# Kernel tuning notes

Measured on AMD Instinct MI355X. Metric: run time of the kernel, lower is better.

## Reference

```python
import jax, jax.numpy as jnp
import numpy as np

N_NUM = 100        # numerical columns
N_CAT = 100        # categorical columns
CAT_COUNT = 100    # categories per categorical column
N_COND = 128
EPS = 1e-5         # torch GroupNorm default eps


def setup_inputs() -> dict:
    key = jax.random.key(0)
    ks = jax.random.split(key, 8)
    B = 4096
    return {
        "x_num": jax.random.normal(ks[0], (B, N_NUM), dtype=jnp.float32),
        "x_cat": jax.random.randint(ks[1], (B, N_CAT), 0, CAT_COUNT),
        "W_num": jax.random.normal(ks[2], (N_NUM, N_COND), dtype=jnp.float32),
        "b_num": jax.random.normal(ks[3], (N_NUM, N_COND), dtype=jnp.float32),
        "emb_table": jax.random.normal(ks[4], (N_CAT * CAT_COUNT, N_COND), dtype=jnp.float32),
        "gn_w": jnp.ones((N_CAT, N_COND), dtype=jnp.float32),
        "gn_b": jnp.zeros((N_CAT, N_COND), dtype=jnp.float32),
        "W_cat": jax.random.normal(ks[5], (N_CAT, N_COND, N_COND), dtype=jnp.float32) / np.sqrt(N_COND).astype(np.float32),
        "b_cat": jax.random.normal(ks[6], (N_CAT, N_COND), dtype=jnp.float32),
    }


def reference(x_num, x_cat, W_num, b_num, emb_table, gn_w, gn_b, W_cat, b_cat):
    # --- numerical branch: grouped 1x1 conv (Cin/g=1, Cout/g=n_cond) + sigmoid ---
    # (B, n_num, 1) * (n_num, n_cond) + bias -> (B, n_num, n_cond)
    num_emb = jax.nn.sigmoid(x_num[:, :, None] * W_num[None] + b_num[None])

    # --- categorical branch ---
    offsets = jnp.arange(N_CAT, dtype=x_cat.dtype) * CAT_COUNT  # cat_offset
    emb = emb_table[x_cat + offsets[None]]  # (B, n_cat, n_cond)

    # GroupNorm with n_cat groups over n_cat*n_cond channels (spatial dim = 1):
    # normalize each column's n_cond features per sample (biased variance).
    mean = jnp.mean(emb, axis=-1, keepdims=True)
    var = jnp.var(emb, axis=-1, keepdims=True)
    normed = (emb - mean) * jax.lax.rsqrt(var + EPS)
    normed = normed * gn_w[None] + gn_b[None]

    # grouped 1x1 conv, groups = n_cat: per-column n_cond x n_cond matmul
    cat_emb = jax.nn.sigmoid(jnp.einsum('bgi,gio->bgo', normed, W_cat) + b_cat[None])

    M = jnp.concatenate([num_emb, cat_emb], axis=1)  # (B, n_num+n_cat, n_cond)
    return jnp.transpose(M, (0, 2, 1))               # (B, n_cond, n_num+n_cat)
```

## Files before the change

kernel.cpp:

```cpp
#include <hip/hip_runtime.h>
#include <cstdint>

#define NNUM 100
#define NCAT 100
#define CATC 100
#define NCOND 128
#define GN_EPS 1e-5f

typedef __attribute__((ext_vector_type(8))) short bfrag8;
typedef __attribute__((ext_vector_type(4))) float accf4;

__device__ __forceinline__ float sigmoidf_(float x) { return 1.0f / (1.0f + __expf(-x)); }

__device__ __forceinline__ ushort f2bf(float f) {
    uint32_t u = __builtin_bit_cast(uint32_t, f);
    u += 0x7fffu + ((u >> 16) & 1u);
    return (ushort)(u >> 16);
}
__device__ __forceinline__ float bf2f(ushort h) {
    return __builtin_bit_cast(float, (uint32_t)h << 16);
}

__global__ __launch_bounds__(256)
void prep_wcat(const float* __restrict__ W_cat, const float* __restrict__ gn_w,
               ushort* __restrict__ Wf)
{
    const int g    = blockIdx.x;
    const int lane = threadIdx.x & 63;
    const int w    = threadIdx.x >> 6;
    const float* Wg = W_cat + ((size_t)g << 14);
    const float* gwg = gn_w + g * NCOND;
    ushort* Wfg = Wf + ((size_t)g << 15);
    #pragma unroll
    for (int i = 0; i < 8; ++i) {
        int p  = w * 8 + i;
        int t  = p >> 2, kk = p & 3;
        int c  = t * 16 + (lane & 15);
        int kb = kk * 32 + ((lane >> 4) << 3);
        ushort hi[8], lo[8];
        #pragma unroll
        for (int j = 0; j < 8; ++j) {
            float v = gwg[kb + j] * Wg[(kb + j) * NCOND + c];
            ushort h = f2bf(v);
            hi[j] = h;
            lo[j] = f2bf(v - bf2f(h));
        }
        int off = ((t * 4 + kk) * 2) * 512 + lane * 8;
        *(bfrag8*)(Wfg + off)       = *(const bfrag8*)hi;
        *(bfrag8*)(Wfg + off + 512) = *(const bfrag8*)lo;
    }
}

__global__ __launch_bounds__(256)
void prep_stats(const float* __restrict__ emb_table, float2* __restrict__ S)
{
    int r = blockIdx.x * 4 + (threadIdx.x >> 6);
    int lane = threadIdx.x & 63;
    if (r >= NCAT * CATC) return;
    const float2* row = (const float2*)(emb_table + ((size_t)r << 7));
    float2 v = row[lane];
    float s  = v.x + v.y;
    float ss = v.x * v.x + v.y * v.y;
    #pragma unroll
    for (int off = 32; off > 0; off >>= 1) {
        s  += __shfl_xor(s,  off, 64);
        ss += __shfl_xor(ss, off, 64);
    }
    float mean = s * 0.0078125f;
    float var  = fmaf(-mean, mean, ss * 0.0078125f);
    float rs   = rsqrtf(var + GN_EPS);
    if (lane == 0) S[r] = make_float2(rs, -mean * rs);
}

__global__ __launch_bounds__(128)
void prep_qp(const float* __restrict__ W_cat, const float* __restrict__ gn_w,
             const float* __restrict__ gn_b, const float* __restrict__ b_cat,
             float* __restrict__ Q, float* __restrict__ P)
{
    const int g = blockIdx.x, o = threadIdx.x;
    const float* Wg = W_cat + ((size_t)g << 14);
    float q = 0.f, p = 0.f;
    #pragma unroll 4
    for (int i = 0; i < NCOND; ++i) {
        float wv = Wg[i * NCOND + o];
        q = fmaf(gn_w[g * NCOND + i], wv, q);
        p = fmaf(gn_b[g * NCOND + i], wv, p);
    }
    Q[g * NCOND + o] = q;
    P[g * NCOND + o] = p + b_cat[g * NCOND + o];
}

__global__ __launch_bounds__(256, 2)
void prep_E_kernel(const float* __restrict__ emb_table,
                   const ushort* __restrict__ Wf,
                   float* __restrict__ E)
{
    const int g    = blockIdx.x;
    const int tid  = threadIdx.x;
    const int lane = tid & 63;
    const int w    = tid >> 6;

    __shared__ __align__(16) ushort Ahi[128 * 128];
    __shared__ __align__(16) ushort Alo[128 * 128];

    const int half = lane >> 5;
    const int l5   = lane & 31;

    #pragma unroll 8
    for (int it = 0; it < 16; ++it) {
        int r = it * 2 + half;
        int m = w * 32 + r;
        int row_id = m < CATC ? m : (CATC - 1);
        const float4* row = (const float4*)(emb_table + ((size_t)(g * CATC + row_id) << 7));
        float4 v = row[l5];
        ushort h0 = f2bf(v.x), h1 = f2bf(v.y), h2 = f2bf(v.z), h3 = f2bf(v.w);
        uint2 hp = { (uint32_t)h0 | ((uint32_t)h1 << 16),
                     (uint32_t)h2 | ((uint32_t)h3 << 16) };
        uint2 lp = { (uint32_t)f2bf(v.x - bf2f(h0)) | ((uint32_t)f2bf(v.y - bf2f(h1)) << 16),
                     (uint32_t)f2bf(v.z - bf2f(h2)) | ((uint32_t)f2bf(v.w - bf2f(h3)) << 16) };
        int bo = m * 256 + ((l5 * 8) ^ ((m & 7) << 4));
        *(uint2*)((char*)Ahi + bo) = hp;
        *(uint2*)((char*)Alo + bo) = lp;
    }
    asm volatile("s_waitcnt lgkmcnt(0)" ::: "memory");

    accf4 acc[2][8];
    #pragma unroll
    for (int gi = 0; gi < 2; ++gi)
        #pragma unroll
        for (int t = 0; t < 8; ++t)
            acc[gi][t] = (accf4){0.f, 0.f, 0.f, 0.f};

    const ushort* Wfg = Wf + ((size_t)g << 15);
    const int row0 = w * 32 + (lane & 15);
    const int sw   = (lane & 7) << 4;

    #pragma unroll
    for (int kk = 0; kk < 4; ++kk) {
        int colb = kk * 64 + ((lane >> 4) << 4);
        int o0 = row0 * 256 + (colb ^ sw);
        int o1 = o0 + 16 * 256;
        bfrag8 ah0 = *(const bfrag8*)((const char*)Ahi + o0);
        bfrag8 al0 = *(const bfrag8*)((const char*)Alo + o0);
        bfrag8 ah1 = *(const bfrag8*)((const char*)Ahi + o1);
        bfrag8 al1 = *(const bfrag8*)((const char*)Alo + o1);
        const ushort* wbase = Wfg + kk * 1024 + lane * 8;
        #pragma unroll
        for (int t = 0; t < 8; ++t) {
            bfrag8 wh = *(const bfrag8*)(wbase + t * 4096);
            bfrag8 wl = *(const bfrag8*)(wbase + t * 4096 + 512);
            acc[0][t] = __builtin_amdgcn_mfma_f32_16x16x32_bf16(ah0, wh, acc[0][t], 0, 0, 0);
            acc[0][t] = __builtin_amdgcn_mfma_f32_16x16x32_bf16(ah0, wl, acc[0][t], 0, 0, 0);
            acc[0][t] = __builtin_amdgcn_mfma_f32_16x16x32_bf16(al0, wh, acc[0][t], 0, 0, 0);
            acc[0][t] = __builtin_amdgcn_mfma_f32_16x16x32_bf16(al0, wl, acc[0][t], 0, 0, 0);
            acc[1][t] = __builtin_amdgcn_mfma_f32_16x16x32_bf16(ah1, wh, acc[1][t], 0, 0, 0);
            acc[1][t] = __builtin_amdgcn_mfma_f32_16x16x32_bf16(ah1, wl, acc[1][t], 0, 0, 0);
            acc[1][t] = __builtin_amdgcn_mfma_f32_16x16x32_bf16(al1, wh, acc[1][t], 0, 0, 0);
            acc[1][t] = __builtin_amdgcn_mfma_f32_16x16x32_bf16(al1, wl, acc[1][t], 0, 0, 0);
        }
    }

    float* Eg = E + (size_t)g * (CATC * NCOND);
    const int colL = lane & 15;
    const int quad = lane >> 4;
    #pragma unroll
    for (int t = 0; t < 8; ++t) {
        int c = t * 16 + colL;
        #pragma unroll
        for (int gi = 0; gi < 2; ++gi) {
            int mbase = (2 * w + gi) * 16 + quad * 4;
            #pragma unroll
            for (int r = 0; r < 4; ++r) {
                int m = mbase + r;
                if (m < CATC) Eg[m * NCOND + c] = acc[gi][t][r];
            }
        }
    }
}

__global__ __launch_bounds__(256)
void transpose_wn(const float* __restrict__ W_num, const float* __restrict__ b_num,
                  float* __restrict__ Wt, float* __restrict__ Bt)
{
    int idx = blockIdx.x * 256 + threadIdx.x;
    if (idx < NCOND * NNUM) {
        int c = idx / NNUM, j = idx - c * NNUM;
        Wt[idx] = W_num[j * NCOND + c];
        Bt[idx] = b_num[j * NCOND + c];
    }
}

__global__ __launch_bounds__(256)
void fused_out_kernel(const int* __restrict__ x_cat,
                      const float* __restrict__ x_num,
                      const float* __restrict__ Wt,
                      const float* __restrict__ Bt,
                      const float* __restrict__ Q,
                      const float* __restrict__ P,
                      const float2* __restrict__ S,
                      const float* __restrict__ E,
                      float* __restrict__ out)
{
    const int b   = blockIdx.x;
    const int h   = blockIdx.y;
    const int tid = threadIdx.x;
    __shared__ float T[NCAT * 65];
    __shared__ float xr[NNUM];
    __shared__ float al[NCAT], be[NCAT];
    __shared__ int   ei[NCAT];

    if (tid < NNUM) xr[tid] = x_num[b * NNUM + tid];
    if (tid < NCAT) {
        int idx = x_cat[(size_t)b * NCAT + tid];
        ei[tid] = idx;
        float2 s2 = S[tid * CATC + idx];
        al[tid] = s2.x;
        be[tid] = s2.y;
    }
    __syncthreads();

    const float4* E4 = (const float4*)E;
    const float4* Q4 = (const float4*)Q;
    const float4* P4 = (const float4*)P;
    #pragma unroll
    for (int it = 0; it < 7; ++it) {
        int i4 = it * 256 + tid;
        if (i4 < NCAT * 16) {
            int g    = i4 >> 4;
            int c4   = i4 & 15;
            int col4 = h * 16 + c4;
            float4 e = E4[(size_t)(g * CATC + ei[g]) * 32 + col4];
            float4 q = Q4[g * 32 + col4];
            float4 p = P4[g * 32 + col4];
            float a = al[g], bb = be[g];
            float* d = &T[g * 65 + c4 * 4];
            d[0] = sigmoidf_(fmaf(a, e.x, fmaf(bb, q.x, p.x)));
            d[1] = sigmoidf_(fmaf(a, e.y, fmaf(bb, q.y, p.y)));
            d[2] = sigmoidf_(fmaf(a, e.z, fmaf(bb, q.z, p.z)));
            d[3] = sigmoidf_(fmaf(a, e.w, fmaf(bb, q.w, p.w)));
        }
    }
    __syncthreads();

    float4* outb = (float4*)(out + (size_t)b * (NCOND * 200)) + h * 3200;
    const float4* Wt4 = (const float4*)Wt;
    const float4* Bt4 = (const float4*)Bt;
    #pragma unroll
    for (int it = 0; it < 13; ++it) {
        int o4 = it * 256 + tid;
        if (o4 < 64 * 50) {
            int c_loc = o4 / 50;
            int j4    = o4 - c_loc * 50;
            int c     = h * 64 + c_loc;
            float4 v;
            if (j4 < 25) {
                float4 wv = Wt4[c * 25 + j4];
                float4 bv = Bt4[c * 25 + j4];
                int j = j4 * 4;
                v.x = sigmoidf_(fmaf(xr[j],     wv.x, bv.x));
                v.y = sigmoidf_(fmaf(xr[j + 1], wv.y, bv.y));
                v.z = sigmoidf_(fmaf(xr[j + 2], wv.z, bv.z));
                v.w = sigmoidf_(fmaf(xr[j + 3], wv.w, bv.w));
            } else {
                int gg = (j4 - 25) * 4;
                v.x = T[(gg    ) * 65 + c_loc];
                v.y = T[(gg + 1) * 65 + c_loc];
                v.z = T[(gg + 2) * 65 + c_loc];
                v.w = T[(gg + 3) * 65 + c_loc];
            }
            outb[o4] = v;
        }
    }
}

extern "C" void kernel_launch(void* const* d_in, const int* in_sizes, int n_in,
                              void* d_out, int out_size, void* d_ws, size_t ws_size,
                              hipStream_t stream)
{
    const float* x_num  = (const float*)d_in[0];
    const int*   x_cat  = (const int*)  d_in[1];
    const float* W_num  = (const float*)d_in[2];
    const float* b_num  = (const float*)d_in[3];
    const float* emb    = (const float*)d_in[4];
    const float* gn_w   = (const float*)d_in[5];
    const float* gn_b   = (const float*)d_in[6];
    const float* W_cat  = (const float*)d_in[7];
    const float* b_cat  = (const float*)d_in[8];
    float* out = (float*)d_out;

    const int B = in_sizes[0] / NNUM;

    float*  Wt = (float*)d_ws;
    float*  Bt = Wt + NCOND * NNUM;
    float*  Qb = Bt + NCOND * NNUM;
    float*  Pb = Qb + NCAT * NCOND;
    float2* Sb = (float2*)(Pb + NCAT * NCOND);
    float*  Eb = (float*)(Sb + NCAT * CATC);
    ushort* Wf = (ushort*)(Eb + NCAT * CATC * NCOND);

    transpose_wn<<<(NCOND * NNUM + 255) / 256, 256, 0, stream>>>(W_num, b_num, Wt, Bt);
    prep_wcat<<<NCAT, 256, 0, stream>>>(W_cat, gn_w, Wf);
    prep_stats<<<(NCAT * CATC + 3) / 4, 256, 0, stream>>>(emb, Sb);
    prep_qp<<<NCAT, 128, 0, stream>>>(W_cat, gn_w, gn_b, b_cat, Qb, Pb);
    prep_E_kernel<<<NCAT, 256, 0, stream>>>(emb, Wf, Eb);
    fused_out_kernel<<<dim3(B, 2), 256, 0, stream>>>(x_cat, x_num, Wt, Bt, Qb, Pb, Sb, Eb, out);
}
```

Measured before the change: 513.4 us.

## Fuse all prep kernels into one and restructure output tile layout

Merges the five preprocessing kernels (W_num transpose, W_cat bf16 split, row stats, Q/P vectors, E matmul) into one launch. The gn_w scaling moves onto the embedding operand, and Q/P come out as two extra MFMA rows, with W_cat split in shared memory in two K-chunks. The output kernel now stores the categorical tile transposed with padding, so the final copy uses float4 shared-memory reads, and it writes numerical and categorical halves in separate loops. This removes several launches and the Wf round trip, at the cost of more per-block work and shared memory in the fused prep kernel.

```diff
diff --git a/kernel.cpp b/kernel.cpp
--- a/kernel.cpp
+++ b/kernel.cpp
@@ -22,141 +22,135 @@
 }
 
 __global__ __launch_bounds__(256)
-void prep_wcat(const float* __restrict__ W_cat, const float* __restrict__ gn_w,
-               ushort* __restrict__ Wf)
+void prep_all(const float* __restrict__ emb_table,
+              const float* __restrict__ W_cat,
+              const float* __restrict__ gn_w,
+              const float* __restrict__ gn_b,
+              const float* __restrict__ b_cat,
+              const float* __restrict__ W_num,
+              const float* __restrict__ b_num,
+              float* __restrict__ E, float* __restrict__ Q, float* __restrict__ P,
+              float2* __restrict__ S,
+              float* __restrict__ Wt, float* __restrict__ Bt)
 {
+    const int tid  = threadIdx.x;
+
+    if (blockIdx.x >= NCAT) {
+        int idx = (blockIdx.x - NCAT) * 256 + tid;
+        if (idx < NCOND * NNUM) {
+            int c = idx / NNUM, j = idx - c * NNUM;
+            Wt[idx] = W_num[j * NCOND + c];
+            Bt[idx] = b_num[j * NCOND + c];
+        }
+        return;
+    }
+
     const int g    = blockIdx.x;
-    const int lane = threadIdx.x & 63;
-    const int w    = threadIdx.x >> 6;
-    const float* Wg = W_cat + ((size_t)g << 14);
-    const float* gwg = gn_w + g * NCOND;
-    ushort* Wfg = Wf + ((size_t)g << 15);
-    #pragma unroll
-    for (int i = 0; i < 8; ++i) {
-        int p  = w * 8 + i;
-        int t  = p >> 2, kk = p & 3;
-        int c  = t * 16 + (lane & 15);
-        int kb = kk * 32 + ((lane >> 4) << 3);
-        ushort hi[8], lo[8];
-        #pragma unroll
-        for (int j = 0; j < 8; ++j) {
-            float v = gwg[kb + j] * Wg[(kb + j) * NCOND + c];
-            ushort h = f2bf(v);
-            hi[j] = h;
-            lo[j] = f2bf(v - bf2f(h));
-        }
-        int off = ((t * 4 + kk) * 2) * 512 + lane * 8;
-        *(bfrag8*)(Wfg + off)       = *(const bfrag8*)hi;
-        *(bfrag8*)(Wfg + off + 512) = *(const bfrag8*)lo;
-    }
-}
-
-__global__ __launch_bounds__(256)
-void prep_stats(const float* __restrict__ emb_table, float2* __restrict__ S)
-{
-    int r = blockIdx.x * 4 + (threadIdx.x >> 6);
-    int lane = threadIdx.x & 63;
-    if (r >= NCAT * CATC) return;
-    const float2* row = (const float2*)(emb_table + ((size_t)r << 7));
-    float2 v = row[lane];
-    float s  = v.x + v.y;
-    float ss = v.x * v.x + v.y * v.y;
-    #pragma unroll
-    for (int off = 32; off > 0; off >>= 1) {
-        s  += __shfl_xor(s,  off, 64);
-        ss += __shfl_xor(ss, off, 64);
-    }
-    float mean = s * 0.0078125f;
-    float var  = fmaf(-mean, mean, ss * 0.0078125f);
-    float rs   = rsqrtf(var + GN_EPS);
-    if (lane == 0) S[r] = make_float2(rs, -mean * rs);
-}
-
-__global__ __launch_bounds__(128)
-void prep_qp(const float* __restrict__ W_cat, const float* __restrict__ gn_w,
-             const float* __restrict__ gn_b, const float* __restrict__ b_cat,
-             float* __restrict__ Q, float* __restrict__ P)
-{
-    const int g = blockIdx.x, o = threadIdx.x;
-    const float* Wg = W_cat + ((size_t)g << 14);
-    float q = 0.f, p = 0.f;
-    #pragma unroll 4
-    for (int i = 0; i < NCOND; ++i) {
-        float wv = Wg[i * NCOND + o];
-        q = fmaf(gn_w[g * NCOND + i], wv, q);
-        p = fmaf(gn_b[g * NCOND + i], wv, p);
-    }
-    Q[g * NCOND + o] = q;
-    P[g * NCOND + o] = p + b_cat[g * NCOND + o];
-}
-
-__global__ __launch_bounds__(256, 2)
-void prep_E_kernel(const float* __restrict__ emb_table,
-                   const ushort* __restrict__ Wf,
-                   float* __restrict__ E)
-{
-    const int g    = blockIdx.x;
-    const int tid  = threadIdx.x;
     const int lane = tid & 63;
     const int w    = tid >> 6;
 
-    __shared__ __align__(16) ushort Ahi[128 * 128];
-    __shared__ __align__(16) ushort Alo[128 * 128];
-
+    __shared__ __align__(16) ushort Ahi[128 * 64];
+    __shared__ __align__(16) ushort Alo[128 * 64];
+    __shared__ __align__(16) ushort Wc[2][8192];
+
+    const float2* emb2 = (const float2*)emb_table;
+    #pragma unroll 5
+    for (int i = 0; i < 25; ++i) {
+        int m = w + 4 * i;
+        float2 v = emb2[(size_t)(g * CATC + m) * 64 + lane];
+        float s  = v.x + v.y;
+        float ss = v.x * v.x + v.y * v.y;
+        #pragma unroll
+        for (int off = 32; off > 0; off >>= 1) {
+            s  += __shfl_xor(s,  off, 64);
+            ss += __shfl_xor(ss, off, 64);
+        }
+        float mean = s * 0.0078125f;
+        float var  = fmaf(-mean, mean, ss * 0.0078125f);
+        float rs   = rsqrtf(var + GN_EPS);
+        if (lane == 0) S[g * CATC + m] = make_float2(rs, -mean * rs);
+    }
+
+    accf4 acc[2][8];
+    #pragma unroll
+    for (int gi = 0; gi < 2; ++gi)
+        #pragma unroll
+        for (int t = 0; t < 8; ++t)
+            acc[gi][t] = (accf4){0.f, 0.f, 0.f, 0.f};
+
+    const float* Wg = W_cat + ((size_t)g << 14);
     const int half = lane >> 5;
     const int l5   = lane & 31;
 
-    #pragma unroll 8
-    for (int it = 0; it < 16; ++it) {
-        int r = it * 2 + half;
-        int m = w * 32 + r;
-        int row_id = m < CATC ? m : (CATC - 1);
-        const float4* row = (const float4*)(emb_table + ((size_t)(g * CATC + row_id) << 7));
-        float4 v = row[l5];
-        ushort h0 = f2bf(v.x), h1 = f2bf(v.y), h2 = f2bf(v.z), h3 = f2bf(v.w);
-        uint2 hp = { (uint32_t)h0 | ((uint32_t)h1 << 16),
-                     (uint32_t)h2 | ((uint32_t)h3 << 16) };
-        uint2 lp = { (uint32_t)f2bf(v.x - bf2f(h0)) | ((uint32_t)f2bf(v.y - bf2f(h1)) << 16),
-                     (uint32_t)f2bf(v.z - bf2f(h2)) | ((uint32_t)f2bf(v.w - bf2f(h3)) << 16) };
-        int bo = m * 256 + ((l5 * 8) ^ ((m & 7) << 4));
-        *(uint2*)((char*)Ahi + bo) = hp;
-        *(uint2*)((char*)Alo + bo) = lp;
-    }
-    asm volatile("s_waitcnt lgkmcnt(0)" ::: "memory");
-
-    accf4 acc[2][8];
-    #pragma unroll
-    for (int gi = 0; gi < 2; ++gi)
-        #pragma unroll
-        for (int t = 0; t < 8; ++t)
-            acc[gi][t] = (accf4){0.f, 0.f, 0.f, 0.f};
-
-    const ushort* Wfg = Wf + ((size_t)g << 15);
-    const int row0 = w * 32 + (lane & 15);
-    const int sw   = (lane & 7) << 4;
-
-    #pragma unroll
-    for (int kk = 0; kk < 4; ++kk) {
-        int colb = kk * 64 + ((lane >> 4) << 4);
-        int o0 = row0 * 256 + (colb ^ sw);
-        int o1 = o0 + 16 * 256;
-        bfrag8 ah0 = *(const bfrag8*)((const char*)Ahi + o0);
-        bfrag8 al0 = *(const bfrag8*)((const char*)Alo + o0);
-        bfrag8 ah1 = *(const bfrag8*)((const char*)Ahi + o1);
-        bfrag8 al1 = *(const bfrag8*)((const char*)Alo + o1);
-        const ushort* wbase = Wfg + kk * 1024 + lane * 8;
-        #pragma unroll
-        for (int t = 0; t < 8; ++t) {
-            bfrag8 wh = *(const bfrag8*)(wbase + t * 4096);
-            bfrag8 wl = *(const bfrag8*)(wbase + t * 4096 + 512);
-            acc[0][t] = __builtin_amdgcn_mfma_f32_16x16x32_bf16(ah0, wh, acc[0][t], 0, 0, 0);
-            acc[0][t] = __builtin_amdgcn_mfma_f32_16x16x32_bf16(ah0, wl, acc[0][t], 0, 0, 0);
-            acc[0][t] = __builtin_amdgcn_mfma_f32_16x16x32_bf16(al0, wh, acc[0][t], 0, 0, 0);
-            acc[0][t] = __builtin_amdgcn_mfma_f32_16x16x32_bf16(al0, wl, acc[0][t], 0, 0, 0);
-            acc[1][t] = __builtin_amdgcn_mfma_f32_16x16x32_bf16(ah1, wh, acc[1][t], 0, 0, 0);
-            acc[1][t] = __builtin_amdgcn_mfma_f32_16x16x32_bf16(ah1, wl, acc[1][t], 0, 0, 0);
-            acc[1][t] = __builtin_amdgcn_mfma_f32_16x16x32_bf16(al1, wh, acc[1][t], 0, 0, 0);
-            acc[1][t] = __builtin_amdgcn_mfma_f32_16x16x32_bf16(al1, wl, acc[1][t], 0, 0, 0);
+    for (int ch = 0; ch < 2; ++ch) {
+        __syncthreads();
+
+        #pragma unroll 2
+        for (int it = 0; it < 8; ++it) {
+            int lin4 = it * 256 + tid;
+            int kl   = lin4 >> 5;
+            int c4   = (lin4 & 31) << 2;
+            float4 v = ((const float4*)Wg)[(ch << 11) + lin4];
+            int kk = kl >> 5, j = kl & 7, lq = ((kl >> 3) & 3) << 4;
+            float vv[4] = {v.x, v.y, v.z, v.w};
+            #pragma unroll
+            for (int e = 0; e < 4; ++e) {
+                int c  = c4 + e;
+                int t  = c >> 4;
+                int lf = (c & 15) | lq;
+                int o  = (((t * 2 + kk) * 64 + lf) << 3) + j;
+                ushort h = f2bf(vv[e]);
+                Wc[0][o] = h;
+                Wc[1][o] = f2bf(vv[e] - bf2f(h));
+            }
+        }
+
+        float2 gw2 = ((const float2*)(gn_w + g * NCOND + ch * 64))[l5];
+        float2 gb2 = ((const float2*)(gn_b + g * NCOND + ch * 64))[l5];
+        #pragma unroll 8
+        for (int it = 0; it < 16; ++it) {
+            int r = it * 2 + half;
+            int m = w * 32 + r;
+            float2 x;
+            if (m < CATC) {
+                float2 v = emb2[(size_t)(g * CATC + m) * 64 + ch * 32 + l5];
+                x.x = v.x * gw2.x; x.y = v.y * gw2.y;
+            } else if (m == CATC)     x = gw2;
+            else if (m == CATC + 1)   x = gb2;
+            else                      x = make_float2(0.f, 0.f);
+            ushort h0 = f2bf(x.x), h1 = f2bf(x.y);
+            uint32_t hp = (uint32_t)h0 | ((uint32_t)h1 << 16);
+            uint32_t lp = (uint32_t)f2bf(x.x - bf2f(h0)) | ((uint32_t)f2bf(x.y - bf2f(h1)) << 16);
+            int bo = m * 128 + ((l5 * 4) ^ ((m & 7) << 4));
+            *(uint32_t*)((char*)Ahi + bo) = hp;
+            *(uint32_t*)((char*)Alo + bo) = lp;
+        }
+        __syncthreads();
+
+        const int row0 = w * 32 + (lane & 15);
+        const int sw   = (lane & 7) << 4;
+        #pragma unroll
+        for (int kk = 0; kk < 2; ++kk) {
+            int colb = kk * 64 + ((lane >> 4) << 4);
+            int o0 = row0 * 128 + (colb ^ sw);
+            int o1 = o0 + 16 * 128;
+            bfrag8 ah0 = *(const bfrag8*)((const char*)Ahi + o0);
+            bfrag8 al0 = *(const bfrag8*)((const char*)Alo + o0);
+            bfrag8 ah1 = *(const bfrag8*)((const char*)Ahi + o1);
+            bfrag8 al1 = *(const bfrag8*)((const char*)Alo + o1);
+            #pragma unroll
+            for (int t = 0; t < 8; ++t) {
+                bfrag8 wh = *(const bfrag8*)&Wc[0][(((t * 2 + kk) * 64 + lane) << 3)];
+                bfrag8 wl = *(const bfrag8*)&Wc[1][(((t * 2 + kk) * 64 + lane) << 3)];
+                acc[0][t] = __builtin_amdgcn_mfma_f32_16x16x32_bf16(ah0, wh, acc[0][t], 0, 0, 0);
+                acc[0][t] = __builtin_amdgcn_mfma_f32_16x16x32_bf16(ah0, wl, acc[0][t], 0, 0, 0);
+                acc[0][t] = __builtin_amdgcn_mfma_f32_16x16x32_bf16(al0, wh, acc[0][t], 0, 0, 0);
+                acc[0][t] = __builtin_amdgcn_mfma_f32_16x16x32_bf16(al0, wl, acc[0][t], 0, 0, 0);
+                acc[1][t] = __builtin_amdgcn_mfma_f32_16x16x32_bf16(ah1, wh, acc[1][t], 0, 0, 0);
+                acc[1][t] = __builtin_amdgcn_mfma_f32_16x16x32_bf16(ah1, wl, acc[1][t], 0, 0, 0);
+                acc[1][t] = __builtin_amdgcn_mfma_f32_16x16x32_bf16(al1, wh, acc[1][t], 0, 0, 0);
+                acc[1][t] = __builtin_amdgcn_mfma_f32_16x16x32_bf16(al1, wl, acc[1][t], 0, 0, 0);
+            }
         }
     }
 
@@ -172,24 +166,16 @@
             #pragma unroll
             for (int r = 0; r < 4; ++r) {
                 int m = mbase + r;
-                if (m < CATC) Eg[m * NCOND + c] = acc[gi][t][r];
+                float val = acc[gi][t][r];
+                if (m < CATC)            Eg[m * NCOND + c] = val;
+                else if (m == CATC)      Q[g * NCOND + c] = val;
+                else if (m == CATC + 1)  P[g * NCOND + c] = val + b_cat[g * NCOND + c];
             }
         }
     }
 }
 
-__global__ __launch_bounds__(256)
-void transpose_wn(const float* __restrict__ W_num, const float* __restrict__ b_num,
-                  float* __restrict__ Wt, float* __restrict__ Bt)
-{
-    int idx = blockIdx.x * 256 + threadIdx.x;
-    if (idx < NCOND * NNUM) {
-        int c = idx / NNUM, j = idx - c * NNUM;
-        Wt[idx] = W_num[j * NCOND + c];
-        Bt[idx] = b_num[j * NCOND + c];
-    }
-}
-
+#define TPAD 108
 __global__ __launch_bounds__(256)
 void fused_out_kernel(const int* __restrict__ x_cat,
                       const float* __restrict__ x_num,
@@ -204,7 +190,7 @@
     const int b   = blockIdx.x;
     const int h   = blockIdx.y;
     const int tid = threadIdx.x;
-    __shared__ float T[NCAT * 65];
+    __shared__ __align__(16) float T[64 * TPAD];
     __shared__ float xr[NNUM];
     __shared__ float al[NCAT], be[NCAT];
     __shared__ int   ei[NCAT];
@@ -233,11 +219,11 @@
             float4 q = Q4[g * 32 + col4];
             float4 p = P4[g * 32 + col4];
             float a = al[g], bb = be[g];
-            float* d = &T[g * 65 + c4 * 4];
-            d[0] = sigmoidf_(fmaf(a, e.x, fmaf(bb, q.x, p.x)));
-            d[1] = sigmoidf_(fmaf(a, e.y, fmaf(bb, q.y, p.y)));
-            d[2] = sigmoidf_(fmaf(a, e.z, fmaf(bb, q.z, p.z)));
-            d[3] = sigmoidf_(fmaf(a, e.w, fmaf(bb, q.w, p.w)));
+            int cl = c4 * 4;
+            T[(cl    ) * TPAD + g] = sigmoidf_(fmaf(a, e.x, fmaf(bb, q.x, p.x)));
+            T[(cl + 1) * TPAD + g] = sigmoidf_(fmaf(a, e.y, fmaf(bb, q.y, p.y)));
+            T[(cl + 2) * TPAD + g] = sigmoidf_(fmaf(a, e.z, fmaf(bb, q.z, p.z)));
+            T[(cl + 3) * TPAD + g] = sigmoidf_(fmaf(a, e.w, fmaf(bb, q.w, p.w)));
         }
     }
     __syncthreads();
@@ -245,30 +231,33 @@
     float4* outb = (float4*)(out + (size_t)b * (NCOND * 200)) + h * 3200;
     const float4* Wt4 = (const float4*)Wt;
     const float4* Bt4 = (const float4*)Bt;
-    #pragma unroll
-    for (int it = 0; it < 13; ++it) {
+
+    #pragma unroll
+    for (int it = 0; it < 7; ++it) {
         int o4 = it * 256 + tid;
-        if (o4 < 64 * 50) {
-            int c_loc = o4 / 50;
-            int j4    = o4 - c_loc * 50;
+        if (o4 < 64 * 25) {
+            int c_loc = o4 / 25;
+            int j4    = o4 - c_loc * 25;
             int c     = h * 64 + c_loc;
+            float4 wv = Wt4[c * 25 + j4];
+            float4 bv = Bt4[c * 25 + j4];
+            int j = j4 * 4;
             float4 v;
-            if (j4 < 25) {
-                float4 wv = Wt4[c * 25 + j4];
-                float4 bv = Bt4[c * 25 + j4];
-                int j = j4 * 4;
-                v.x = sigmoidf_(fmaf(xr[j],     wv.x, bv.x));
-                v.y = sigmoidf_(fmaf(xr[j + 1], wv.y, bv.y));
-                v.z = sigmoidf_(fmaf(xr[j + 2], wv.z, bv.z));
-                v.w = sigmoidf_(fmaf(xr[j + 3], wv.w, bv.w));
-            } else {
-                int gg = (j4 - 25) * 4;
-                v.x = T[(gg    ) * 65 + c_loc];
-                v.y = T[(gg + 1) * 65 + c_loc];
-                v.z = T[(gg + 2) * 65 + c_loc];
-                v.w = T[(gg + 3) * 65 + c_loc];
-            }
-            outb[o4] = v;
+            v.x = sigmoidf_(fmaf(xr[j],     wv.x, bv.x));
+            v.y = sigmoidf_(fmaf(xr[j + 1], wv.y, bv.y));
+            v.z = sigmoidf_(fmaf(xr[j + 2], wv.z, bv.z));
+            v.w = sigmoidf_(fmaf(xr[j + 3], wv.w, bv.w));
+            outb[c_loc * 50 + j4] = v;
+        }
+    }
+    #pragma unroll
+    for (int it = 0; it < 7; ++it) {
+        int o4 = it * 256 + tid;
+        if (o4 < 64 * 25) {
+            int c_loc = o4 / 25;
+            int g4    = o4 - c_loc * 25;
+            float4 v = *(const float4*)&T[c_loc * TPAD + g4 * 4];
+            outb[c_loc * 50 + 25 + g4] = v;
         }
     }
 }
@@ -296,12 +285,8 @@
     float*  Pb = Qb + NCAT * NCOND;
     float2* Sb = (float2*)(Pb + NCAT * NCOND);
     float*  Eb = (float*)(Sb + NCAT * CATC);
-    ushort* Wf = (ushort*)(Eb + NCAT * CATC * NCOND);
-
-    transpose_wn<<<(NCOND * NNUM + 255) / 256, 256, 0, stream>>>(W_num, b_num, Wt, Bt);
-    prep_wcat<<<NCAT, 256, 0, stream>>>(W_cat, gn_w, Wf);
-    prep_stats<<<(NCAT * CATC + 3) / 4, 256, 0, stream>>>(emb, Sb);
-    prep_qp<<<NCAT, 128, 0, stream>>>(W_cat, gn_w, gn_b, b_cat, Qb, Pb);
-    prep_E_kernel<<<NCAT, 256, 0, stream>>>(emb, Wf, Eb);
+
+    prep_all<<<NCAT + 50, 256, 0, stream>>>(emb, W_cat, gn_w, gn_b, b_cat,
+                                            W_num, b_num, Eb, Qb, Pb, Sb, Wt, Bt);
     fused_out_kernel<<<dim3(B, 2), 256, 0, stream>>>(x_cat, x_num, Wt, Bt, Qb, Pb, Sb, Eb, out);
 }
```

New measurement: 549.2 us. 1.07x slower.

## Merge prep kernels, fold Q/P into MFMA tile, split E over column halves

Applied to the files above, without the earlier changes.

Three small prep kernels (W_num transpose, W_cat bf16 split, emb row stats) become one launch. The Q/P reduction is removed: gn_w and gn_b go into the padding rows 100 and 101 of the MFMA A tile, and gn_w is applied to the embedding rows instead of to W_cat. prep_E now runs two blocks per group, each doing half of the output columns, which doubles parallelism but loads each group's embedding tile twice. The output kernel stores T transposed so the categorical half is written with float4 LDS reads in its own loop, and sigmoid now uses the fast reciprocal.

```diff
diff --git a/kernel.cpp b/kernel.cpp
--- a/kernel.cpp
+++ b/kernel.cpp
@@ -10,7 +10,9 @@
 typedef __attribute__((ext_vector_type(8))) short bfrag8;
 typedef __attribute__((ext_vector_type(4))) float accf4;
 
-__device__ __forceinline__ float sigmoidf_(float x) { return 1.0f / (1.0f + __expf(-x)); }
+__device__ __forceinline__ float sigmoidf_(float x) {
+    return __builtin_amdgcn_rcpf(1.0f + __expf(-x));
+}
 
 __device__ __forceinline__ ushort f2bf(float f) {
     uint32_t u = __builtin_bit_cast(uint32_t, f);
@@ -22,113 +24,119 @@
 }
 
 __global__ __launch_bounds__(256)
-void prep_wcat(const float* __restrict__ W_cat, const float* __restrict__ gn_w,
-               ushort* __restrict__ Wf)
+void prep_misc(const float* __restrict__ emb_table,
+               const float* __restrict__ W_cat,
+               const float* __restrict__ W_num,
+               const float* __restrict__ b_num,
+               ushort* __restrict__ Wf,
+               float2* __restrict__ S,
+               float* __restrict__ Wt, float* __restrict__ Bt)
 {
-    const int g    = blockIdx.x;
-    const int lane = threadIdx.x & 63;
-    const int w    = threadIdx.x >> 6;
-    const float* Wg = W_cat + ((size_t)g << 14);
-    const float* gwg = gn_w + g * NCOND;
-    ushort* Wfg = Wf + ((size_t)g << 15);
-    #pragma unroll
-    for (int i = 0; i < 8; ++i) {
-        int p  = w * 8 + i;
-        int t  = p >> 2, kk = p & 3;
-        int c  = t * 16 + (lane & 15);
-        int kb = kk * 32 + ((lane >> 4) << 3);
-        ushort hi[8], lo[8];
-        #pragma unroll
-        for (int j = 0; j < 8; ++j) {
-            float v = gwg[kb + j] * Wg[(kb + j) * NCOND + c];
-            ushort h = f2bf(v);
-            hi[j] = h;
-            lo[j] = f2bf(v - bf2f(h));
-        }
-        int off = ((t * 4 + kk) * 2) * 512 + lane * 8;
-        *(bfrag8*)(Wfg + off)       = *(const bfrag8*)hi;
-        *(bfrag8*)(Wfg + off + 512) = *(const bfrag8*)lo;
-    }
-}
-
-__global__ __launch_bounds__(256)
-void prep_stats(const float* __restrict__ emb_table, float2* __restrict__ S)
-{
-    int r = blockIdx.x * 4 + (threadIdx.x >> 6);
-    int lane = threadIdx.x & 63;
-    if (r >= NCAT * CATC) return;
-    const float2* row = (const float2*)(emb_table + ((size_t)r << 7));
-    float2 v = row[lane];
-    float s  = v.x + v.y;
-    float ss = v.x * v.x + v.y * v.y;
-    #pragma unroll
-    for (int off = 32; off > 0; off >>= 1) {
-        s  += __shfl_xor(s,  off, 64);
-        ss += __shfl_xor(ss, off, 64);
-    }
-    float mean = s * 0.0078125f;
-    float var  = fmaf(-mean, mean, ss * 0.0078125f);
-    float rs   = rsqrtf(var + GN_EPS);
-    if (lane == 0) S[r] = make_float2(rs, -mean * rs);
-}
-
-__global__ __launch_bounds__(128)
-void prep_qp(const float* __restrict__ W_cat, const float* __restrict__ gn_w,
-             const float* __restrict__ gn_b, const float* __restrict__ b_cat,
-             float* __restrict__ Q, float* __restrict__ P)
-{
-    const int g = blockIdx.x, o = threadIdx.x;
-    const float* Wg = W_cat + ((size_t)g << 14);
-    float q = 0.f, p = 0.f;
-    #pragma unroll 4
-    for (int i = 0; i < NCOND; ++i) {
-        float wv = Wg[i * NCOND + o];
-        q = fmaf(gn_w[g * NCOND + i], wv, q);
-        p = fmaf(gn_b[g * NCOND + i], wv, p);
-    }
-    Q[g * NCOND + o] = q;
-    P[g * NCOND + o] = p + b_cat[g * NCOND + o];
-}
-
-__global__ __launch_bounds__(256, 2)
-void prep_E_kernel(const float* __restrict__ emb_table,
-                   const ushort* __restrict__ Wf,
-                   float* __restrict__ E)
-{
-    const int g    = blockIdx.x;
+    const int bid  = blockIdx.x;
     const int tid  = threadIdx.x;
     const int lane = tid & 63;
     const int w    = tid >> 6;
 
+    if (bid < NCAT) {
+        const int g = bid;
+        const float* Wg = W_cat + ((size_t)g << 14);
+        ushort* Wfg = Wf + ((size_t)g << 15);
+        #pragma unroll
+        for (int i = 0; i < 8; ++i) {
+            int p  = w * 8 + i;
+            int t  = p >> 2, kk = p & 3;
+            int c  = t * 16 + (lane & 15);
+            int kb = kk * 32 + ((lane >> 4) << 3);
+            ushort hi[8], lo[8];
+            #pragma unroll
+            for (int j = 0; j < 8; ++j) {
+                float v = Wg[(kb + j) * NCOND + c];
+                ushort h = f2bf(v);
+                hi[j] = h;
+                lo[j] = f2bf(v - bf2f(h));
+            }
+            int off = ((t * 4 + kk) * 2) * 512 + lane * 8;
+            *(bfrag8*)(Wfg + off)       = *(const bfrag8*)hi;
+            *(bfrag8*)(Wfg + off + 512) = *(const bfrag8*)lo;
+        }
+    } else if (bid < NCAT + 50) {
+        int idx = (bid - NCAT) * 256 + tid;
+        if (idx < NCOND * NNUM) {
+            int c = idx / NNUM, j = idx - c * NNUM;
+            Wt[idx] = W_num[j * NCOND + c];
+            Bt[idx] = b_num[j * NCOND + c];
+        }
+    } else {
+        int r = (bid - NCAT - 50) * 4 + w;
+        if (r < NCAT * CATC) {
+            const float2* row = (const float2*)(emb_table + ((size_t)r << 7));
+            float2 v = row[lane];
+            float s  = v.x + v.y;
+            float ss = v.x * v.x + v.y * v.y;
+            #pragma unroll
+            for (int off = 32; off > 0; off >>= 1) {
+                s  += __shfl_xor(s,  off, 64);
+                ss += __shfl_xor(ss, off, 64);
+            }
+            float mean = s * 0.0078125f;
+            float var  = fmaf(-mean, mean, ss * 0.0078125f);
+            float rs   = rsqrtf(var + GN_EPS);
+            if (lane == 0) S[r] = make_float2(rs, -mean * rs);
+        }
+    }
+}
+
+__global__ __launch_bounds__(256, 2)
+void prep_E_kernel(const float* __restrict__ emb_table,
+                   const float* __restrict__ gn_w,
+                   const float* __restrict__ gn_b,
+                   const float* __restrict__ b_cat,
+                   const ushort* __restrict__ Wf,
+                   float* __restrict__ E, float* __restrict__ Q, float* __restrict__ P)
+{
+    const int g    = blockIdx.x;
+    const int h    = blockIdx.y;
+    const int tid  = threadIdx.x;
+    const int lane = tid & 63;
+    const int w    = tid >> 6;
+
     __shared__ __align__(16) ushort Ahi[128 * 128];
     __shared__ __align__(16) ushort Alo[128 * 128];
 
     const int half = lane >> 5;
     const int l5   = lane & 31;
+    float4 gwv = *(const float4*)(gn_w + g * NCOND + l5 * 4);
+    float4 gbv = *(const float4*)(gn_b + g * NCOND + l5 * 4);
 
     #pragma unroll 8
     for (int it = 0; it < 16; ++it) {
         int r = it * 2 + half;
         int m = w * 32 + r;
-        int row_id = m < CATC ? m : (CATC - 1);
-        const float4* row = (const float4*)(emb_table + ((size_t)(g * CATC + row_id) << 7));
-        float4 v = row[l5];
-        ushort h0 = f2bf(v.x), h1 = f2bf(v.y), h2 = f2bf(v.z), h3 = f2bf(v.w);
+        float4 x;
+        if (m < CATC) {
+            const float4* row = (const float4*)(emb_table + ((size_t)(g * CATC + m) << 7));
+            float4 v = row[l5];
+            x.x = v.x * gwv.x; x.y = v.y * gwv.y;
+            x.z = v.z * gwv.z; x.w = v.w * gwv.w;
+        } else if (m == CATC)     x = gwv;
+        else if (m == CATC + 1)   x = gbv;
+        else                      x = make_float4(0.f, 0.f, 0.f, 0.f);
+        ushort h0 = f2bf(x.x), h1 = f2bf(x.y), h2 = f2bf(x.z), h3 = f2bf(x.w);
         uint2 hp = { (uint32_t)h0 | ((uint32_t)h1 << 16),
                      (uint32_t)h2 | ((uint32_t)h3 << 16) };
-        uint2 lp = { (uint32_t)f2bf(v.x - bf2f(h0)) | ((uint32_t)f2bf(v.y - bf2f(h1)) << 16),
-                     (uint32_t)f2bf(v.z - bf2f(h2)) | ((uint32_t)f2bf(v.w - bf2f(h3)) << 16) };
+        uint2 lp = { (uint32_t)f2bf(x.x - bf2f(h0)) | ((uint32_t)f2bf(x.y - bf2f(h1)) << 16),
+                     (uint32_t)f2bf(x.z - bf2f(h2)) | ((uint32_t)f2bf(x.w - bf2f(h3)) << 16) };
         int bo = m * 256 + ((l5 * 8) ^ ((m & 7) << 4));
         *(uint2*)((char*)Ahi + bo) = hp;
         *(uint2*)((char*)Alo + bo) = lp;
     }
     asm volatile("s_waitcnt lgkmcnt(0)" ::: "memory");
 
-    accf4 acc[2][8];
+    accf4 acc[2][4];
     #pragma unroll
     for (int gi = 0; gi < 2; ++gi)
         #pragma unroll
-        for (int t = 0; t < 8; ++t)
+        for (int t = 0; t < 4; ++t)
             acc[gi][t] = (accf4){0.f, 0.f, 0.f, 0.f};
 
     const ushort* Wfg = Wf + ((size_t)g << 15);
@@ -146,17 +154,18 @@
         bfrag8 al1 = *(const bfrag8*)((const char*)Alo + o1);
         const ushort* wbase = Wfg + kk * 1024 + lane * 8;
         #pragma unroll
-        for (int t = 0; t < 8; ++t) {
+        for (int tt = 0; tt < 4; ++tt) {
+            int t = h * 4 + tt;
             bfrag8 wh = *(const bfrag8*)(wbase + t * 4096);
             bfrag8 wl = *(const bfrag8*)(wbase + t * 4096 + 512);
-            acc[0][t] = __builtin_amdgcn_mfma_f32_16x16x32_bf16(ah0, wh, acc[0][t], 0, 0, 0);
-            acc[0][t] = __builtin_amdgcn_mfma_f32_16x16x32_bf16(ah0, wl, acc[0][t], 0, 0, 0);
-            acc[0][t] = __builtin_amdgcn_mfma_f32_16x16x32_bf16(al0, wh, acc[0][t], 0, 0, 0);
-            acc[0][t] = __builtin_amdgcn_mfma_f32_16x16x32_bf16(al0, wl, acc[0][t], 0, 0, 0);
-            acc[1][t] = __builtin_amdgcn_mfma_f32_16x16x32_bf16(ah1, wh, acc[1][t], 0, 0, 0);
-            acc[1][t] = __builtin_amdgcn_mfma_f32_16x16x32_bf16(ah1, wl, acc[1][t], 0, 0, 0);
-            acc[1][t] = __builtin_amdgcn_mfma_f32_16x16x32_bf16(al1, wh, acc[1][t], 0, 0, 0);
-            acc[1][t] = __builtin_amdgcn_mfma_f32_16x16x32_bf16(al1, wl, acc[1][t], 0, 0, 0);
+            acc[0][tt] = __builtin_amdgcn_mfma_f32_16x16x32_bf16(ah0, wh, acc[0][tt], 0, 0, 0);
+            acc[0][tt] = __builtin_amdgcn_mfma_f32_16x16x32_bf16(ah0, wl, acc[0][tt], 0, 0, 0);
+            acc[0][tt] = __builtin_amdgcn_mfma_f32_16x16x32_bf16(al0, wh, acc[0][tt], 0, 0, 0);
+            acc[0][tt] = __builtin_amdgcn_mfma_f32_16x16x32_bf16(al0, wl, acc[0][tt], 0, 0, 0);
+            acc[1][tt] = __builtin_amdgcn_mfma_f32_16x16x32_bf16(ah1, wh, acc[1][tt], 0, 0, 0);
+            acc[1][tt] = __builtin_amdgcn_mfma_f32_16x16x32_bf16(ah1, wl, acc[1][tt], 0, 0, 0);
+            acc[1][tt] = __builtin_amdgcn_mfma_f32_16x16x32_bf16(al1, wh, acc[1][tt], 0, 0, 0);
+            acc[1][tt] = __builtin_amdgcn_mfma_f32_16x16x32_bf16(al1, wl, acc[1][tt], 0, 0, 0);
         }
     }
 
@@ -164,32 +173,24 @@
     const int colL = lane & 15;
     const int quad = lane >> 4;
     #pragma unroll
-    for (int t = 0; t < 8; ++t) {
-        int c = t * 16 + colL;
+    for (int tt = 0; tt < 4; ++tt) {
+        int c = (h * 4 + tt) * 16 + colL;
         #pragma unroll
         for (int gi = 0; gi < 2; ++gi) {
             int mbase = (2 * w + gi) * 16 + quad * 4;
             #pragma unroll
             for (int r = 0; r < 4; ++r) {
                 int m = mbase + r;
-                if (m < CATC) Eg[m * NCOND + c] = acc[gi][t][r];
+                float val = acc[gi][tt][r];
+                if (m < CATC)            Eg[m * NCOND + c] = val;
+                else if (m == CATC)      Q[g * NCOND + c] = val;
+                else if (m == CATC + 1)  P[g * NCOND + c] = val + b_cat[g * NCOND + c];
             }
         }
     }
 }
 
-__global__ __launch_bounds__(256)
-void transpose_wn(const float* __restrict__ W_num, const float* __restrict__ b_num,
-                  float* __restrict__ Wt, float* __restrict__ Bt)
-{
-    int idx = blockIdx.x * 256 + threadIdx.x;
-    if (idx < NCOND * NNUM) {
-        int c = idx / NNUM, j = idx - c * NNUM;
-        Wt[idx] = W_num[j * NCOND + c];
-        Bt[idx] = b_num[j * NCOND + c];
-    }
-}
-
+#define TPAD 108
 __global__ __launch_bounds__(256)
 void fused_out_kernel(const int* __restrict__ x_cat,
                       const float* __restrict__ x_num,
@@ -204,7 +205,7 @@
     const int b   = blockIdx.x;
     const int h   = blockIdx.y;
     const int tid = threadIdx.x;
-    __shared__ float T[NCAT * 65];
+    __shared__ __align__(16) float T[64 * TPAD];
     __shared__ float xr[NNUM];
     __shared__ float al[NCAT], be[NCAT];
     __shared__ int   ei[NCAT];
@@ -233,11 +234,11 @@
             float4 q = Q4[g * 32 + col4];
             float4 p = P4[g * 32 + col4];
             float a = al[g], bb = be[g];
-            float* d = &T[g * 65 + c4 * 4];
-            d[0] = sigmoidf_(fmaf(a, e.x, fmaf(bb, q.x, p.x)));
-            d[1] = sigmoidf_(fmaf(a, e.y, fmaf(bb, q.y, p.y)));
-            d[2] = sigmoidf_(fmaf(a, e.z, fmaf(bb, q.z, p.z)));
-            d[3] = sigmoidf_(fmaf(a, e.w, fmaf(bb, q.w, p.w)));
+            int cl = c4 * 4;
+            T[(cl    ) * TPAD + g] = sigmoidf_(fmaf(a, e.x, fmaf(bb, q.x, p.x)));
+            T[(cl + 1) * TPAD + g] = sigmoidf_(fmaf(a, e.y, fmaf(bb, q.y, p.y)));
+            T[(cl + 2) * TPAD + g] = sigmoidf_(fmaf(a, e.z, fmaf(bb, q.z, p.z)));
+            T[(cl + 3) * TPAD + g] = sigmoidf_(fmaf(a, e.w, fmaf(bb, q.w, p.w)));
         }
     }
     __syncthreads();
@@ -245,30 +246,33 @@
     float4* outb = (float4*)(out + (size_t)b * (NCOND * 200)) + h * 3200;
     const float4* Wt4 = (const float4*)Wt;
     const float4* Bt4 = (const float4*)Bt;
-    #pragma unroll
-    for (int it = 0; it < 13; ++it) {
+
+    #pragma unroll
+    for (int it = 0; it < 7; ++it) {
         int o4 = it * 256 + tid;
-        if (o4 < 64 * 50) {
-            int c_loc = o4 / 50;
-            int j4    = o4 - c_loc * 50;
+        if (o4 < 64 * 25) {
+            int c_loc = o4 / 25;
+            int j4    = o4 - c_loc * 25;
             int c     = h * 64 + c_loc;
+            float4 wv = Wt4[c * 25 + j4];
+            float4 bv = Bt4[c * 25 + j4];
+            int j = j4 * 4;
             float4 v;
-            if (j4 < 25) {
-                float4 wv = Wt4[c * 25 + j4];
-                float4 bv = Bt4[c * 25 + j4];
-                int j = j4 * 4;
-                v.x = sigmoidf_(fmaf(xr[j],     wv.x, bv.x));
-                v.y = sigmoidf_(fmaf(xr[j + 1], wv.y, bv.y));
-                v.z = sigmoidf_(fmaf(xr[j + 2], wv.z, bv.z));
-                v.w = sigmoidf_(fmaf(xr[j + 3], wv.w, bv.w));
-            } else {
-                int gg = (j4 - 25) * 4;
-                v.x = T[(gg    ) * 65 + c_loc];
-                v.y = T[(gg + 1) * 65 + c_loc];
-                v.z = T[(gg + 2) * 65 + c_loc];
-                v.w = T[(gg + 3) * 65 + c_loc];
-            }
-            outb[o4] = v;
+            v.x = sigmoidf_(fmaf(xr[j],     wv.x, bv.x));
+            v.y = sigmoidf_(fmaf(xr[j + 1], wv.y, bv.y));
+            v.z = sigmoidf_(fmaf(xr[j + 2], wv.z, bv.z));
+            v.w = sigmoidf_(fmaf(xr[j + 3], wv.w, bv.w));
+            outb[c_loc * 50 + j4] = v;
+        }
+    }
+    #pragma unroll
+    for (int it = 0; it < 7; ++it) {
+        int o4 = it * 256 + tid;
+        if (o4 < 64 * 25) {
+            int c_loc = o4 / 25;
+            int g4    = o4 - c_loc * 25;
+            float4 v = *(const float4*)&T[c_loc * TPAD + g4 * 4];
+            outb[c_loc * 50 + 25 + g4] = v;
         }
     }
 }
@@ -298,10 +302,10 @@
     float*  Eb = (float*)(Sb + NCAT * CATC);
     ushort* Wf = (ushort*)(Eb + NCAT * CATC * NCOND);
 
-    transpose_wn<<<(NCOND * NNUM + 255) / 256, 256, 0, stream>>>(W_num, b_num, Wt, Bt);
-    prep_wcat<<<NCAT, 256, 0, stream>>>(W_cat, gn_w, Wf);
-    prep_stats<<<(NCAT * CATC + 3) / 4, 256, 0, stream>>>(emb, Sb);
-    prep_qp<<<NCAT, 128, 0, stream>>>(W_cat, gn_w, gn_b, b_cat, Qb, Pb);
-    prep_E_kernel<<<NCAT, 256, 0, stream>>>(emb, Wf, Eb);
-    fused_out_kernel<<<dim3(B, 2), 256, 0, stream>>>(x_cat, x_num, Wt, Bt, Qb, Pb, Sb, Eb, out);
-}
+    prep_misc<<<NCAT + 50 + (NCAT * CATC + 3) / 4, 256, 0, stream>>>(
+        emb, W_cat, W_num, b_num, Wf, Sb, Wt, Bt);
+    prep_E_kernel<<<dim3(NCAT, 2), 256, 0, stream>>>(
+        emb, gn_w, gn_b, b_cat, Wf, Eb, Qb, Pb);
+    fused_out_kernel<<<dim3(B, 2), 256, 0, stream>>>(
+        x_cat, x_num, Wt, Bt, Qb, Pb, Sb, Eb, out);
+}
```

New measurement: 525.1 us. 1.02x slower.
